# Kernel tuning notes

Hardware: AMD Instinct MI355X
Metric: run time of the kernel (lower is better)

The kernel has to match this reference:

```python
import jax, jax.numpy as jnp
import numpy as np

B, C, H, W_ = 64, 768, 24, 24
POOL = 4  # pool_size
HID = 768


def setup_inputs() -> dict:
    key = jax.random.key(0)
    ks = jax.random.split(key, 12)
    search_feat = jax.random.normal(ks[0], (B, C, H, W_), dtype=jnp.float32)
    # valid normalized boxes (x0,y0,x1,y1) in [0,1]
    cx = jax.random.uniform(ks[1], (B,), minval=0.25, maxval=0.75)
    cy = jax.random.uniform(ks[2], (B,), minval=0.25, maxval=0.75)
    bw = jax.random.uniform(ks[3], (B,), minval=0.1, maxval=0.5)
    bh = jax.random.uniform(ks[4], (B,), minval=0.1, maxval=0.5)
    x0 = jnp.clip(cx - bw / 2, 0.0, 1.0)
    x1 = jnp.clip(cx + bw / 2, 0.0, 1.0)
    y0 = jnp.clip(cy - bh / 2, 0.0, 1.0)
    y1 = jnp.clip(cy + bh / 2, 0.0, 1.0)
    search_box = jnp.stack([x0, y0, x1, y1], axis=1).astype(jnp.float32)
    sc = 0.02
    w1 = jax.random.normal(ks[5], (C, HID), dtype=jnp.float32) * sc
    b1 = jnp.zeros((HID,), jnp.float32)
    w2 = jax.random.normal(ks[6], (HID, HID), dtype=jnp.float32) * sc
    b2 = jnp.zeros((HID,), jnp.float32)
    w3 = jax.random.normal(ks[7], (HID, 1), dtype=jnp.float32) * sc
    b3 = jnp.zeros((1,), jnp.float32)
    return dict(search_feat=search_feat, search_box=search_box,
                w1=w1, b1=b1, w2=w2, b2=b2, w3=w3, b3=b3)


def _hat_cdf(t):
    # CDF of the triangular (bilinear) kernel tri(u)=max(0,1-|u|):
    # F(t) = integral_{-inf}^{t} tri(u) du
    return jnp.where(t <= -1.0, 0.0,
           jnp.where(t <= 0.0, 0.5 * (t + 1.0) ** 2,
           jnpp := jnp.where(t <= 1.0, 1.0 - 0.5 * (1.0 - t) ** 2, 1.0)))


def _bin_weights(lo, hi, n):
    # lo, hi: [B, P] bin edges in continuous pixel coords.
    # Returns [B, P, n]: integral of hat centered at each integer pixel over [lo, hi].
    c = jnp.arange(n, dtype=lo.dtype)
    return _hat_cdf(hi[..., None] - c) - _hat_cdf(lo[..., None] - c)


def reference(search_feat, search_box, w1, b1, w2, b2, w3, b3):
    b, c, h, w = search_feat.shape
    box = search_box * w  # module scales normalized coords by feature width
    x0, y0, x1, y1 = box[:, 0], box[:, 1], box[:, 2], box[:, 3]
    bw = (x1 - x0) / POOL  # per-roi bin width
    bh = (y1 - y0) / POOL
    i = jnp.arange(POOL, dtype=box.dtype)
    ex_lo = x0[:, None] + i * bw[:, None]   # [B, P]
    ex_hi = ex_lo + bw[:, None]
    ey_lo = y0[:, None] + i * bh[:, None]
    ey_hi = ey_lo + bh[:, None]
    # PrRoIPool: exact integral of bilinearly-interpolated feature over each bin.
    # Bilinear interp is a separable hat-basis expansion (zero outside the map),
    # so the 2D integral factors into per-axis weights.
    Wx = _bin_weights(ex_lo, ex_hi, w)      # [B, P, W]
    Wy = _bin_weights(ey_lo, ey_hi, h)      # [B, P, H]
    raw = jnp.einsum('bph,bchw,bqw->bcpq', Wy, search_feat, Wx)
    area = (bw * bh)[:, None, None, None]
    pooled = jnp.where(area > 0, raw / jnp.maximum(area, 1e-12), 0.0)  # [B,C,P,P]
    # rearrange 'b c h w -> b (h w) c' then AdaptiveAvgPool1d(1) over tokens
    feat = jnp.mean(pooled, axis=(2, 3))[:, None, :]  # [B, 1, C]
    x = jax.nn.relu(feat @ w1 + b1)
    x = jax.nn.relu(x @ w2 + b2)
    out = x @ w3 + b3                                  # [B, 1, 1]
    return out
```

## Files before the change

kernel.cpp:

```cpp
#include <hip/hip_runtime.h>

#define B_DIM 64
#define C_DIM 768
#define HID_DIM 768
#define PLANE 576
#define PLANE4 144
#define KCH 96
#define OT 64

__device__ __forceinline__ float hatcdf(float t) {
    float u = fminf(fmaxf(t, -1.f), 1.f);
    float a = u + 1.f;
    float b = 1.f - u;
    return (t <= 0.f) ? 0.5f * a * a : 1.f - 0.5f * b * b;
}

__global__ __launch_bounds__(256) void pool_kernel(
    const float* __restrict__ X, const float* __restrict__ box,
    float* __restrict__ feat, float* __restrict__ zbuf)
{
    const int t = threadIdx.x;
    const int bx = blockIdx.x;
    if (bx < 96) {
        reinterpret_cast<float4*>(zbuf)[bx * 256 + t] = make_float4(0.f, 0.f, 0.f, 0.f);
    }

    const int b = bx >> 5;
    __shared__ float wx[24], wy[24];
    __shared__ float sscale;
    if (t < 49) {
        const float x0 = box[b * 4 + 0] * 24.f;
        const float y0 = box[b * 4 + 1] * 24.f;
        const float x1 = box[b * 4 + 2] * 24.f;
        const float y1 = box[b * 4 + 3] * 24.f;
        if (t < 24) {
            wx[t] = hatcdf(x1 - (float)t) - hatcdf(x0 - (float)t);
        } else if (t < 48) {
            const int h = t - 24;
            wy[h] = hatcdf(y1 - (float)h) - hatcdf(y0 - (float)h);
        } else {
            const float bw = (x1 - x0) * 0.25f;
            const float bh = (y1 - y0) * 0.25f;
            const float area = bw * bh;
            sscale = (area > 0.f) ? 1.f / (16.f * fmaxf(area, 1e-12f)) : 0.f;
        }
    }
    __syncthreads();

    const int wave = t >> 6;
    const int lane = t & 63;
    const int c0 = (bx & 31) * 24 + wave * 6;
    const float4* __restrict__ P =
        reinterpret_cast<const float4*>(X + ((size_t)b * C_DIM + c0) * PLANE);

    float acc[6];
    #pragma unroll
    for (int r = 0; r < 6; ++r) acc[r] = 0.f;

    #pragma unroll
    for (int r = 0; r < 6; ++r) {
        const float4* __restrict__ Q = P + r * PLANE4;
        int f = lane;
        float4 v = Q[f];
        int h = f / 6, wb = (f - h * 6) * 4;
        acc[r] += wy[h] * (v.x * wx[wb] + v.y * wx[wb + 1] + v.z * wx[wb + 2] + v.w * wx[wb + 3]);
        f = lane + 64;
        v = Q[f];
        h = f / 6; wb = (f - h * 6) * 4;
        acc[r] += wy[h] * (v.x * wx[wb] + v.y * wx[wb + 1] + v.z * wx[wb + 2] + v.w * wx[wb + 3]);
        if (lane < 16) {
            f = lane + 128;
            v = Q[f];
            h = f / 6; wb = (f - h * 6) * 4;
            acc[r] += wy[h] * (v.x * wx[wb] + v.y * wx[wb + 1] + v.z * wx[wb + 2] + v.w * wx[wb + 3]);
        }
    }

    #pragma unroll
    for (int r = 0; r < 6; ++r) {
        float a = acc[r];
        #pragma unroll
        for (int off = 32; off; off >>= 1) a += __shfl_down(a, off);
        if (lane == 0) feat[(size_t)b * C_DIM + c0 + r] = a * sscale;
    }
}

template <bool RELU_IN>
__global__ __launch_bounds__(256) void fc_chunk(
    const float* __restrict__ A, const float* __restrict__ bias,
    const float* __restrict__ Wm, float* __restrict__ Out)
{
    __shared__ float As[KCH][68];
    __shared__ float Ws[KCH][68];
    const int t = threadIdx.x;
    const int ot = blockIdx.x * OT;
    const int kc = blockIdx.y * KCH;

    for (int j = t; j < B_DIM * (KCH / 4); j += 256) {
        const int bb = j / (KCH / 4);
        const int k4 = (j % (KCH / 4)) * 4;
        float4 v = *reinterpret_cast<const float4*>(A + (size_t)bb * HID_DIM + kc + k4);
        if constexpr (RELU_IN) {
            const float4 bv = *reinterpret_cast<const float4*>(bias + kc + k4);
            v.x = fmaxf(v.x + bv.x, 0.f);
            v.y = fmaxf(v.y + bv.y, 0.f);
            v.z = fmaxf(v.z + bv.z, 0.f);
            v.w = fmaxf(v.w + bv.w, 0.f);
        }
        As[k4 + 0][bb] = v.x;
        As[k4 + 1][bb] = v.y;
        As[k4 + 2][bb] = v.z;
        As[k4 + 3][bb] = v.w;
    }
    for (int j = t; j < KCH * (OT / 4); j += 256) {
        const int k = j / (OT / 4);
        const int oo = (j % (OT / 4)) * 4;
        const float4 v = *reinterpret_cast<const float4*>(Wm + (size_t)(kc + k) * HID_DIM + ot + oo);
        *reinterpret_cast<float4*>(&Ws[k][oo]) = v;
    }
    __syncthreads();

    const int b0 = (t >> 4) * 4;
    const int o0 = (t & 15) * 4;
    float acc[4][4] = {};
    #pragma unroll 4
    for (int k = 0; k < KCH; ++k) {
        const float4 a = *reinterpret_cast<const float4*>(&As[k][b0]);
        const float4 w = *reinterpret_cast<const float4*>(&Ws[k][o0]);
        acc[0][0] += a.x * w.x; acc[0][1] += a.x * w.y; acc[0][2] += a.x * w.z; acc[0][3] += a.x * w.w;
        acc[1][0] += a.y * w.x; acc[1][1] += a.y * w.y; acc[1][2] += a.y * w.z; acc[1][3] += a.y * w.w;
        acc[2][0] += a.z * w.x; acc[2][1] += a.z * w.y; acc[2][2] += a.z * w.z; acc[2][3] += a.z * w.w;
        acc[3][0] += a.w * w.x; acc[3][1] += a.w * w.y; acc[3][2] += a.w * w.z; acc[3][3] += a.w * w.w;
    }
    #pragma unroll
    for (int i = 0; i < 4; ++i)
        #pragma unroll
        for (int j = 0; j < 4; ++j)
            atomicAdd(&Out[(size_t)(b0 + i) * HID_DIM + ot + o0 + j], acc[i][j]);
}

__global__ __launch_bounds__(256) void head_kernel(
    const float* __restrict__ x2raw, const float* __restrict__ b2,
    const float* __restrict__ w3, const float* __restrict__ b3,
    float* __restrict__ out)
{
    const int b = blockIdx.x;
    const int t = threadIdx.x;
    float acc = 0.f;
    for (int o = t; o < HID_DIM; o += 256)
        acc += fmaxf(x2raw[(size_t)b * HID_DIM + o] + b2[o], 0.f) * w3[o];
    #pragma unroll
    for (int off = 32; off; off >>= 1) acc += __shfl_down(acc, off);
    __shared__ float r[4];
    if ((t & 63) == 0) r[t >> 6] = acc;
    __syncthreads();
    if (t == 0) out[b] = r[0] + r[1] + r[2] + r[3] + b3[0];
}

extern "C" void kernel_launch(void* const* d_in, const int* in_sizes, int n_in,
                              void* d_out, int out_size, void* d_ws, size_t ws_size,
                              hipStream_t stream) {
    const float* X   = (const float*)d_in[0];
    const float* box = (const float*)d_in[1];
    const float* w1  = (const float*)d_in[2];
    const float* b1  = (const float*)d_in[3];
    const float* w2  = (const float*)d_in[4];
    const float* b2  = (const float*)d_in[5];
    const float* w3  = (const float*)d_in[6];
    const float* b3  = (const float*)d_in[7];
    float* out = (float*)d_out;

    float* feat  = (float*)d_ws;
    float* x1raw = feat + B_DIM * HID_DIM;
    float* x2raw = x1raw + B_DIM * HID_DIM;

    pool_kernel<<<2048, 256, 0, stream>>>(X, box, feat, x1raw);
    fc_chunk<false><<<dim3(HID_DIM / OT, HID_DIM / KCH), 256, 0, stream>>>(feat, b1, w1, x1raw);
    fc_chunk<true><<<dim3(HID_DIM / OT, HID_DIM / KCH), 256, 0, stream>>>(x1raw, b1, w2, x2raw);
    head_kernel<<<B_DIM, 256, 0, stream>>>(x2raw, b2, w3, b3, out);
}
```

Before: 213.2 us.

## Fuse MLP layers and head into one per-batch kernel without atomics

Replaces the two split-K FC kernels (which accumulate with atomics) and the separate head kernel with a single kernel. It runs one 768-thread block per batch row, keeps the hidden activations in shared memory and ends with a block reduction for the head. This removes two launches, the buffer zeroing inside the pool kernel, and all atomic traffic. The cost is that each of only 64 blocks streams both full weight matrices through cache, so the MLP uses few CUs and depends on per-CU cache bandwidth.

```diff
diff --git a/kernel.cpp b/kernel.cpp
--- a/kernel.cpp
+++ b/kernel.cpp
@@ -5,8 +5,6 @@
 #define HID_DIM 768
 #define PLANE 576
 #define PLANE4 144
-#define KCH 96
-#define OT 64
 
 __device__ __forceinline__ float hatcdf(float t) {
     float u = fminf(fmaxf(t, -1.f), 1.f);
@@ -17,15 +15,12 @@
 
 __global__ __launch_bounds__(256) void pool_kernel(
     const float* __restrict__ X, const float* __restrict__ box,
-    float* __restrict__ feat, float* __restrict__ zbuf)
+    float* __restrict__ feat)
 {
     const int t = threadIdx.x;
     const int bx = blockIdx.x;
-    if (bx < 96) {
-        reinterpret_cast<float4*>(zbuf)[bx * 256 + t] = make_float4(0.f, 0.f, 0.f, 0.f);
-    }
+    const int b = bx >> 5;
 
-    const int b = bx >> 5;
     __shared__ float wx[24], wy[24];
     __shared__ float sscale;
     if (t < 49) {
@@ -85,76 +80,60 @@
     }
 }
 
-template <bool RELU_IN>
-__global__ __launch_bounds__(256) void fc_chunk(
-    const float* __restrict__ A, const float* __restrict__ bias,
-    const float* __restrict__ Wm, float* __restrict__ Out)
-{
-    __shared__ float As[KCH][68];
-    __shared__ float Ws[KCH][68];
-    const int t = threadIdx.x;
-    const int ot = blockIdx.x * OT;
-    const int kc = blockIdx.y * KCH;
-
-    for (int j = t; j < B_DIM * (KCH / 4); j += 256) {
-        const int bb = j / (KCH / 4);
-        const int k4 = (j % (KCH / 4)) * 4;
-        float4 v = *reinterpret_cast<const float4*>(A + (size_t)bb * HID_DIM + kc + k4);
-        if constexpr (RELU_IN) {
-            const float4 bv = *reinterpret_cast<const float4*>(bias + kc + k4);
-            v.x = fmaxf(v.x + bv.x, 0.f);
-            v.y = fmaxf(v.y + bv.y, 0.f);
-            v.z = fmaxf(v.z + bv.z, 0.f);
-            v.w = fmaxf(v.w + bv.w, 0.f);
-        }
-        As[k4 + 0][bb] = v.x;
-        As[k4 + 1][bb] = v.y;
-        As[k4 + 2][bb] = v.z;
-        As[k4 + 3][bb] = v.w;
-    }
-    for (int j = t; j < KCH * (OT / 4); j += 256) {
-        const int k = j / (OT / 4);
-        const int oo = (j % (OT / 4)) * 4;
-        const float4 v = *reinterpret_cast<const float4*>(Wm + (size_t)(kc + k) * HID_DIM + ot + oo);
-        *reinterpret_cast<float4*>(&Ws[k][oo]) = v;
-    }
-    __syncthreads();
-
-    const int b0 = (t >> 4) * 4;
-    const int o0 = (t & 15) * 4;
-    float acc[4][4] = {};
-    #pragma unroll 4
-    for (int k = 0; k < KCH; ++k) {
-        const float4 a = *reinterpret_cast<const float4*>(&As[k][b0]);
-        const float4 w = *reinterpret_cast<const float4*>(&Ws[k][o0]);
-        acc[0][0] += a.x * w.x; acc[0][1] += a.x * w.y; acc[0][2] += a.x * w.z; acc[0][3] += a.x * w.w;
-        acc[1][0] += a.y * w.x; acc[1][1] += a.y * w.y; acc[1][2] += a.y * w.z; acc[1][3] += a.y * w.w;
-        acc[2][0] += a.z * w.x; acc[2][1] += a.z * w.y; acc[2][2] += a.z * w.z; acc[2][3] += a.z * w.w;
-        acc[3][0] += a.w * w.x; acc[3][1] += a.w * w.y; acc[3][2] += a.w * w.z; acc[3][3] += a.w * w.w;
-    }
-    #pragma unroll
-    for (int i = 0; i < 4; ++i)
-        #pragma unroll
-        for (int j = 0; j < 4; ++j)
-            atomicAdd(&Out[(size_t)(b0 + i) * HID_DIM + ot + o0 + j], acc[i][j]);
-}
-
-__global__ __launch_bounds__(256) void head_kernel(
-    const float* __restrict__ x2raw, const float* __restrict__ b2,
+__global__ __launch_bounds__(768) void mlp_kernel(
+    const float* __restrict__ feat,
+    const float* __restrict__ w1, const float* __restrict__ b1,
+    const float* __restrict__ w2, const float* __restrict__ b2,
     const float* __restrict__ w3, const float* __restrict__ b3,
     float* __restrict__ out)
 {
     const int b = blockIdx.x;
     const int t = threadIdx.x;
-    float acc = 0.f;
-    for (int o = t; o < HID_DIM; o += 256)
-        acc += fmaxf(x2raw[(size_t)b * HID_DIM + o] + b2[o], 0.f) * w3[o];
+    __shared__ float fs[HID_DIM];
+    __shared__ float x1s[HID_DIM];
+    __shared__ float r[12];
+
+    if (t < HID_DIM / 4) {
+        reinterpret_cast<float4*>(fs)[t] =
+            reinterpret_cast<const float4*>(feat + (size_t)b * HID_DIM)[t];
+    }
+    __syncthreads();
+
+    float acc = b1[t];
+    for (int k = 0; k < HID_DIM; k += 8) {
+        float wv[8];
+        #pragma unroll
+        for (int j = 0; j < 8; ++j)
+            wv[j] = w1[(size_t)(k + j) * HID_DIM + t];
+        #pragma unroll
+        for (int j = 0; j < 8; ++j)
+            acc += fs[k + j] * wv[j];
+    }
+    x1s[t] = fmaxf(acc, 0.f);
+    __syncthreads();
+
+    float acc2 = b2[t];
+    for (int k = 0; k < HID_DIM; k += 8) {
+        float wv[8];
+        #pragma unroll
+        for (int j = 0; j < 8; ++j)
+            wv[j] = w2[(size_t)(k + j) * HID_DIM + t];
+        #pragma unroll
+        for (int j = 0; j < 8; ++j)
+            acc2 += x1s[k + j] * wv[j];
+    }
+    float p = fmaxf(acc2, 0.f) * w3[t];
+
     #pragma unroll
-    for (int off = 32; off; off >>= 1) acc += __shfl_down(acc, off);
-    __shared__ float r[4];
-    if ((t & 63) == 0) r[t >> 6] = acc;
+    for (int off = 32; off; off >>= 1) p += __shfl_down(p, off);
+    if ((t & 63) == 0) r[t >> 6] = p;
     __syncthreads();
-    if (t == 0) out[b] = r[0] + r[1] + r[2] + r[3] + b3[0];
+    if (t == 0) {
+        float s = b3[0];
+        #pragma unroll
+        for (int i = 0; i < 12; ++i) s += r[i];
+        out[b] = s;
+    }
 }
 
 extern "C" void kernel_launch(void* const* d_in, const int* in_sizes, int n_in,
@@ -170,12 +149,8 @@
     const float* b3  = (const float*)d_in[7];
     float* out = (float*)d_out;
 
-    float* feat  = (float*)d_ws;
-    float* x1raw = feat + B_DIM * HID_DIM;
-    float* x2raw = x1raw + B_DIM * HID_DIM;
+    float* feat = (float*)d_ws;
 
-    pool_kernel<<<2048, 256, 0, stream>>>(X, box, feat, x1raw);
-    fc_chunk<false><<<dim3(HID_DIM / OT, HID_DIM / KCH), 256, 0, stream>>>(feat, b1, w1, x1raw);
-    fc_chunk<true><<<dim3(HID_DIM / OT, HID_DIM / KCH), 256, 0, stream>>>(x1raw, b1, w2, x2raw);
-    head_kernel<<<B_DIM, 256, 0, stream>>>(x2raw, b2, w3, b3, out);
+    pool_kernel<<<2048, 256, 0, stream>>>(X, box, feat);
+    mlp_kernel<<<B_DIM, 768, 0, stream>>>(feat, w1, b1, w2, b2, w3, b3, out);
 }
```

Result: slower. 248.6 us (+16.6%).
